# Performance work log

Hardware: AMD Instinct MI355X
Metric: run time of the kernel (lower is better)

The kernel has to match this reference:

```python
import jax, jax.numpy as jnp
import numpy as np

V = 778   # MANO mesh vertex count (hard-coded in the module)
K = 9     # spiral neighborhood length
C = 256   # in_channels
OUT = 3   # out_channels (per-vertex offset xyz)
B3 = 192  # 3 * B, B = 64


def setup_inputs() -> dict:
    key = jax.random.key(0)
    ks = jax.random.split(key, 12)
    x = jax.random.normal(ks[0], (B3, V, C), jnp.float32)
    pred_occ = jax.random.normal(ks[1], (B3, 2, 5), jnp.float32)
    indices = jax.random.randint(ks[2], (V, K), 0, V)
    finger_sizes = [112, 120, 124, 116, 108]
    fingers = {f"finger{i}": jax.random.randint(ks[3 + i], (n,), 0, V)
               for i, n in enumerate(finger_sizes)}

    def lin(k, fan_in, fan_out):
        kw, kb = jax.random.split(k)
        w = jax.random.normal(kw, (fan_in, fan_out), jnp.float32) / np.float32(np.sqrt(fan_in))
        b = jax.random.normal(kb, (fan_out,), jnp.float32) * 0.01
        return w, b

    w0, b0 = lin(ks[8], 2 * C * K, 2 * C)
    w1, b1 = lin(ks[9], 2 * C * K, C)
    w2, b2 = lin(ks[10], C * K, C)
    wh, bh = lin(ks[11], C * K, OUT)
    return {"x": x, "pred_occ": pred_occ, "indices": indices, **fingers,
            "w0": w0, "b0": b0, "w1": w1, "b1": b1, "w2": w2, "b2": b2,
            "wh": wh, "bh": bh}


def spiral_conv(x, idx, w, b):
    # x: [B, V, Cin], idx: [V, K] -> gather spiral neighbors, flatten, linear
    B = x.shape[0]
    g = x[:, idx.reshape(-1), :].reshape(B, V, -1)  # [B, V, K*Cin]
    return g @ w + b


def reference(x, pred_occ, indices, finger0, finger1, finger2, finger3, finger4,
              w0, b0, w1, b1, w2, b2, wh, bh):
    # Per-finger non-occlusion probabilities: softmax over class dim, take class 0
    occ = jax.nn.softmax(pred_occ, axis=1)[:, 0, :5]          # [3B, 5]
    weights = jnp.ones((x.shape[0], V), x.dtype)
    for i, fidx in enumerate([finger0, finger1, finger2, finger3, finger4]):
        val = jnp.broadcast_to(occ[:, i:i + 1], (x.shape[0], fidx.shape[0]))
        weights = weights.at[:, fidx].set(val)
    B = x.shape[0] // 3
    wv = jnp.stack(jnp.split(weights, 3, axis=0), axis=-1)[..., None]  # [B, V, 3, 1]
    wv = jax.nn.softmax(wv, axis=2)
    xv = jnp.stack(jnp.split(x, 3, axis=0), axis=2)                    # [B, V, 3, C]
    wx = jnp.sum(wv * xv, axis=2)                                      # [B, V, C]
    h = jnp.concatenate([wx, x[:B]], axis=2)                           # [B, V, 2C]
    h = jax.nn.relu(spiral_conv(h, indices, w0, b0))
    h = jax.nn.relu(spiral_conv(h, indices, w1, b1))
    h = jax.nn.relu(spiral_conv(h, indices, w2, b2))
    return spiral_conv(h, indices, wh, bh)                             # [B, V, 3]
```

## Files before the change

### kernel.cpp

```cpp
#include <hip/hip_runtime.h>

typedef unsigned short ushort_t;
typedef __attribute__((ext_vector_type(8))) __bf16 bf16x8;
typedef __attribute__((ext_vector_type(8))) unsigned short ushort8;
typedef __attribute__((ext_vector_type(4))) float floatx4;
typedef __attribute__((ext_vector_type(16))) float floatx16;

#define VN 778
#define KNB 9

__device__ __forceinline__ float bf2f(unsigned short s) {
  union { unsigned int u; float f; } x; x.u = ((unsigned int)s) << 16; return x.f;
}
__device__ __forceinline__ unsigned short f2bf(float f) {
  union { float f; unsigned int u; } x; x.f = f;
  unsigned int r = x.u + 0x7fffu + ((x.u >> 16) & 1u);
  return (unsigned short)(r >> 16);
}

__global__ void prep_misc(const float* __restrict__ pred_occ,
                          const int* f0, const int* f1, const int* f2,
                          const int* f3, const int* f4,
                          int n0, int n1, int n2, int n3, int n4,
                          const float* __restrict__ wh,
                          float* __restrict__ occ, int* __restrict__ fid,
                          float* __restrict__ whT) {
  int t = threadIdx.x;
  for (int i = t; i < 192 * 5; i += 256) {
    int r = i / 5, f = i % 5;
    float p0 = pred_occ[r * 10 + f];
    float p1 = pred_occ[r * 10 + 5 + f];
    occ[i] = 1.0f / (1.0f + __expf(p1 - p0));
  }
  for (int i = t; i < VN; i += 256) fid[i] = -1;
  __syncthreads();
  const int* fp[5] = {f0, f1, f2, f3, f4};
  int fn[5] = {n0, n1, n2, n3, n4};
  for (int fi = 0; fi < 5; ++fi) {
    for (int i = t; i < fn[fi]; i += 256) fid[fp[fi][i]] = fi;
    __syncthreads();
  }
  for (int i = t; i < 3 * 2304; i += 256) {
    int o = i / 2304, k = i % 2304;
    whT[i] = wh[k * 3 + o];
  }
}

__global__ void wx_kernel(const float* __restrict__ x, const float* __restrict__ occ,
                          const int* __restrict__ fid, ushort_t* __restrict__ wx) {
  int g = blockIdx.x * 256 + threadIdx.x;
  int c8 = (g & 31) << 3;
  int bv = g >> 5;
  int b = bv / VN;
  int v = bv - b * VN;
  int f = fid[v];
  float w0 = 1.f, w1 = 1.f, w2 = 1.f;
  if (f >= 0) {
    w0 = occ[b * 5 + f];
    w1 = occ[(64 + b) * 5 + f];
    w2 = occ[(128 + b) * 5 + f];
  }
  float m = fmaxf(w0, fmaxf(w1, w2));
  float e0 = __expf(w0 - m), e1 = __expf(w1 - m), e2 = __expf(w2 - m);
  float inv = 1.0f / (e0 + e1 + e2);
  e0 *= inv; e1 *= inv; e2 *= inv;
  size_t base = (size_t)bv * 256 + c8;
  const size_t V1 = (size_t)64 * VN * 256, V2 = (size_t)128 * VN * 256;
  floatx4 x0a = *(const floatx4*)(x + base);
  floatx4 x0b = *(const floatx4*)(x + base + 4);
  floatx4 x1a = *(const floatx4*)(x + V1 + base);
  floatx4 x1b = *(const floatx4*)(x + V1 + base + 4);
  floatx4 x2a = *(const floatx4*)(x + V2 + base);
  floatx4 x2b = *(const floatx4*)(x + V2 + base + 4);
  ushort8 o;
#pragma unroll
  for (int e = 0; e < 4; ++e) {
    o[e]     = f2bf(e0 * x0a[e] + e1 * x1a[e] + e2 * x2a[e]);
    o[e + 4] = f2bf(e0 * x0b[e] + e1 * x1b[e] + e2 * x2b[e]);
  }
  *(ushort8*)(wx + base) = o;
}

__global__ void pack_w(const float* __restrict__ w, ushort_t* __restrict__ wP,
                       int N, int ksn, int total) {
  int chunk = blockIdx.x * 256 + threadIdx.x;
  if (chunk >= total) return;
  int lane = chunk & 63;
  int rest = chunk >> 6;
  int ks = rest % ksn;
  int tn = rest / ksn;
  int n = (tn << 5) + (lane & 31);
  int kb = (ks << 4) + ((lane >> 5) << 3);
  ushort8 o;
#pragma unroll
  for (int j = 0; j < 8; ++j) o[j] = f2bf(w[(size_t)(kb + j) * N + n]);
  *(ushort8*)(wP + (size_t)chunk * 8) = o;
}

template <int CIN, bool SPLIT>
__global__ __launch_bounds__(512, 4) void spiral_gemm(
    const ushort_t* __restrict__ act0, const float* __restrict__ actF,
    const ushort_t* __restrict__ wP, const float* __restrict__ bias,
    const int* __restrict__ idx, ushort_t* __restrict__ out, int NOUT) {
  constexpr int PHASES = CIN / 128;
  __shared__ __align__(16) ushort_t Alds[2 * 64 * 128];
  const int v0 = blockIdx.x * 2;
  const int n0 = blockIdx.y << 8;
  const int tid = threadIdx.x;
  const int lane = tid & 63;
  const int wv = tid >> 6;
  const int vi = wv >> 2;
  const int nq = wv & 3;
  const int mlo = lane & 31;
  const int q = lane >> 5;
  const int xm = mlo & 7;
  floatx16 acc00{}, acc01{}, acc10{}, acc11{};
  const int KtotSteps = KNB * (CIN / 16);
  const int tn0 = (n0 >> 5) + (nq << 1);
  const ushort_t* bp0 = wP + (size_t)tn0 * KtotSteps * 512 + lane * 8;
  const ushort_t* bp1 = bp0 + (size_t)KtotSteps * 512;
  const int* iv0 = idx + v0 * KNB;
  const int* iv1 = idx + (v0 + 1) * KNB;
  const int a_off0 = vi * 64 * 128 + mlo * 128;
  const int a_off1 = vi * 64 * 128 + (mlo + 32) * 128;
  for (int nbr = 0; nbr < KNB; ++nbr) {
    const int nv0 = iv0[nbr], nv1 = iv1[nbr];
#pragma unroll
    for (int h = 0; h < PHASES; ++h) {
      __syncthreads();
#pragma unroll
      for (int it = 0; it < 4; ++it) {
        int L = it * 512 + tid;
        int ck = L & 15;
        int row = (L >> 4) & 63;
        int vv = L >> 10;
        int nv = vv ? nv1 : nv0;
        int c = ck << 3;
        ushort8 val;
        if (SPLIT && h >= 2) {
          const float* src = actF + ((size_t)(row * VN + nv)) * 256 + (h - 2) * 128 + c;
          floatx4 fa = *(const floatx4*)src;
          floatx4 fb = *(const floatx4*)(src + 4);
#pragma unroll
          for (int e = 0; e < 4; ++e) { val[e] = f2bf(fa[e]); val[e + 4] = f2bf(fb[e]); }
        } else {
          const ushort_t* src = act0 + ((size_t)(row * VN + nv)) * (SPLIT ? 256 : CIN)
                                + h * 128 + c;
          val = *(const ushort8*)src;
        }
        int slot = ck ^ (row & 7);
        *(ushort8*)&Alds[(size_t)(vv * 64 * 128) + (size_t)(row * 16 + slot) * 8] = val;
      }
      __syncthreads();
#pragma unroll
      for (int ks = 0; ks < 8; ++ks) {
        int ck0 = ((ks << 1) + q) ^ xm;
        bf16x8 a0 = *(const bf16x8*)&Alds[a_off0 + ck0 * 8];
        bf16x8 a1 = *(const bf16x8*)&Alds[a_off1 + ck0 * 8];
        bf16x8 b0v = *(const bf16x8*)bp0; bp0 += 512;
        bf16x8 b1v = *(const bf16x8*)bp1; bp1 += 512;
        acc00 = __builtin_amdgcn_mfma_f32_32x32x16_bf16(a0, b0v, acc00, 0, 0, 0);
        acc10 = __builtin_amdgcn_mfma_f32_32x32x16_bf16(a1, b0v, acc10, 0, 0, 0);
        acc01 = __builtin_amdgcn_mfma_f32_32x32x16_bf16(a0, b1v, acc01, 0, 0, 0);
        acc11 = __builtin_amdgcn_mfma_f32_32x32x16_bf16(a1, b1v, acc11, 0, 0, 0);
      }
    }
  }
  const int v = v0 + vi;
  const int na = n0 + (nq << 6) + mlo;
  const int nb = na + 32;
  const float ba = bias[na];
  const float bb = bias[nb];
#pragma unroll
  for (int r = 0; r < 16; ++r) {
    int m = (r & 3) + ((r >> 2) << 3) + (q << 2);
    size_t o0 = ((size_t)(m * VN + v)) * NOUT;
    size_t o1 = ((size_t)((m + 32) * VN + v)) * NOUT;
    float v00 = acc00[r] + ba; v00 = v00 > 0.f ? v00 : 0.f;
    float v01 = acc01[r] + bb; v01 = v01 > 0.f ? v01 : 0.f;
    float v10 = acc10[r] + ba; v10 = v10 > 0.f ? v10 : 0.f;
    float v11 = acc11[r] + bb; v11 = v11 > 0.f ? v11 : 0.f;
    out[o0 + na] = f2bf(v00);
    out[o0 + nb] = f2bf(v01);
    out[o1 + na] = f2bf(v10);
    out[o1 + nb] = f2bf(v11);
  }
}

__global__ void head_kernel(const ushort_t* __restrict__ act, const float* __restrict__ whT,
                            const float* __restrict__ bh, const int* __restrict__ idx,
                            float* __restrict__ out) {
  __shared__ __align__(16) ushort_t Alds[64 * 256];
  const int v = blockIdx.x;
  const int tid = threadIdx.x;
  float a0 = 0.f, a1 = 0.f, a2 = 0.f;
  const int b = tid;
  const int xm = b & 7;
  for (int nbr = 0; nbr < KNB; ++nbr) {
    const int nv = idx[v * KNB + nbr];
    __syncthreads();
#pragma unroll
    for (int it = 0; it < 8; ++it) {
      int L = it * 256 + tid;
      int bb = L >> 5;
      int jj = L & 31;
      ushort8 val = *(const ushort8*)(act + ((size_t)(bb * VN + nv)) * 256 + (jj << 3));
      int slot = jj ^ (bb & 7);
      *(ushort8*)&Alds[(size_t)(bb * 32 + slot) * 8] = val;
    }
    __syncthreads();
    if (tid < 64) {
      const float* wp = whT + nbr * 256;
#pragma unroll 4
      for (int j = 0; j < 32; ++j) {
        int jj = j ^ xm;
        ushort8 a8 = *(const ushort8*)&Alds[(b * 32 + jj) * 8];
#pragma unroll
        for (int e = 0; e < 8; ++e) {
          float av = bf2f(a8[e]);
          int k = (j << 3) + e;
          a0 += av * wp[k];
          a1 += av * wp[2304 + k];
          a2 += av * wp[4608 + k];
        }
      }
    }
  }
  if (tid < 64) {
    size_t o = ((size_t)(b * VN + v)) * 3;
    out[o + 0] = a0 + bh[0];
    out[o + 1] = a1 + bh[1];
    out[o + 2] = a2 + bh[2];
  }
}

extern "C" void kernel_launch(void* const* d_in, const int* in_sizes, int n_in,
                              void* d_out, int out_size, void* d_ws, size_t ws_size,
                              hipStream_t stream) {
  const float* x        = (const float*)d_in[0];
  const float* pred_occ = (const float*)d_in[1];
  const int* indices    = (const int*)d_in[2];
  const int* f0 = (const int*)d_in[3];
  const int* f1 = (const int*)d_in[4];
  const int* f2 = (const int*)d_in[5];
  const int* f3 = (const int*)d_in[6];
  const int* f4 = (const int*)d_in[7];
  const float* w0 = (const float*)d_in[8];
  const float* b0 = (const float*)d_in[9];
  const float* w1 = (const float*)d_in[10];
  const float* b1 = (const float*)d_in[11];
  const float* w2 = (const float*)d_in[12];
  const float* b2 = (const float*)d_in[13];
  const float* wh = (const float*)d_in[14];
  const float* bh = (const float*)d_in[15];
  float* outp = (float*)d_out;

  char* ws = (char*)d_ws;
  ushort_t* wP0 = (ushort_t*)(ws + 0);
  ushort_t* wP1 = (ushort_t*)(ws + 4718592);
  ushort_t* wP2 = (ushort_t*)(ws + 7077888);
  float* whT    = (float*)(ws + 8257536);
  float* occ    = (float*)(ws + 8285184);
  int* fid      = (int*)(ws + 8289024);
  ushort_t* R0  = (ushort_t*)(ws + 8292352);
  ushort_t* R1  = (ushort_t*)(ws + 33785856);

  prep_misc<<<1, 256, 0, stream>>>(pred_occ, f0, f1, f2, f3, f4,
                                   in_sizes[3], in_sizes[4], in_sizes[5],
                                   in_sizes[6], in_sizes[7], wh, occ, fid, whT);
  pack_w<<<294912 / 256, 256, 0, stream>>>(w0, wP0, 512, 288, 294912);
  pack_w<<<147456 / 256, 256, 0, stream>>>(w1, wP1, 256, 288, 147456);
  pack_w<<<73728 / 256, 256, 0, stream>>>(w2, wP2, 256, 144, 73728);
  wx_kernel<<<6224, 256, 0, stream>>>(x, occ, fid, R0);

  dim3 g0(VN / 2, 2), g1(VN / 2, 1);
  spiral_gemm<512, true><<<g0, 512, 0, stream>>>(R0, x, wP0, b0, indices, R1, 512);
  spiral_gemm<512, false><<<g1, 512, 0, stream>>>(R1, nullptr, wP1, b1, indices, R0, 256);
  spiral_gemm<256, false><<<g1, 512, 0, stream>>>(R0, nullptr, wP2, b2, indices, R1, 256);
  head_kernel<<<VN, 256, 0, stream>>>(R1, whT, bh, indices, outp);
  (void)n_in; (void)out_size; (void)ws_size;
}
```

Baseline: 1.0000 ms.

## Double-buffer spiral GEMM with direct global-to-LDS loads and pre-converted bf16 input

```diff
diff --git a/kernel.cpp b/kernel.cpp
--- a/kernel.cpp
+++ b/kernel.cpp
@@ -16,6 +16,12 @@
   union { float f; unsigned int u; } x; x.f = f;
   unsigned int r = x.u + 0x7fffu + ((x.u >> 16) & 1u);
   return (unsigned short)(r >> 16);
+}
+
+__device__ __forceinline__ void load_lds16(const void* g, void* l) {
+  __builtin_amdgcn_global_load_lds(
+      (const __attribute__((address_space(1))) unsigned int*)g,
+      (__attribute__((address_space(3))) unsigned int*)l, 16, 0, 0);
 }
 
 __global__ void prep_misc(const float* __restrict__ pred_occ,
@@ -81,6 +87,17 @@
   *(ushort8*)(wx + base) = o;
 }
 
+__global__ void xcvt_kernel(const float* __restrict__ x, ushort_t* __restrict__ xb) {
+  int g = blockIdx.x * 256 + threadIdx.x;
+  size_t base = (size_t)g * 8;
+  floatx4 fa = *(const floatx4*)(x + base);
+  floatx4 fb = *(const floatx4*)(x + base + 4);
+  ushort8 o;
+#pragma unroll
+  for (int e = 0; e < 4; ++e) { o[e] = f2bf(fa[e]); o[e + 4] = f2bf(fb[e]); }
+  *(ushort8*)(xb + base) = o;
+}
+
 __global__ void pack_w(const float* __restrict__ w, ushort_t* __restrict__ wP,
                        int N, int ksn, int total) {
   int chunk = blockIdx.x * 256 + threadIdx.x;
@@ -97,93 +114,113 @@
   *(ushort8*)(wP + (size_t)chunk * 8) = o;
 }
 
-template <int CIN, bool SPLIT>
+template <int CIN, int MODE>
 __global__ __launch_bounds__(512, 4) void spiral_gemm(
     const ushort_t* __restrict__ act0, const float* __restrict__ actF,
-    const ushort_t* __restrict__ wP, const float* __restrict__ bias,
-    const int* __restrict__ idx, ushort_t* __restrict__ out, int NOUT) {
-  constexpr int PHASES = CIN / 128;
-  __shared__ __align__(16) ushort_t Alds[2 * 64 * 128];
+    const ushort_t* __restrict__ actB, const ushort_t* __restrict__ wP,
+    const float* __restrict__ bias, const int* __restrict__ idx,
+    ushort_t* __restrict__ out, int NOUT) {
+  constexpr int H = CIN / 128;
+  constexpr int P = KNB * H;
+  __shared__ __align__(16) ushort_t Alds[2][2048 * 8];
   const int v0 = blockIdx.x * 2;
   const int n0 = blockIdx.y << 8;
   const int tid = threadIdx.x;
   const int lane = tid & 63;
   const int wv = tid >> 6;
-  const int vi = wv >> 2;
-  const int nq = wv & 3;
   const int mlo = lane & 31;
   const int q = lane >> 5;
   const int xm = mlo & 7;
-  floatx16 acc00{}, acc01{}, acc10{}, acc11{};
+  floatx16 acc0{}, acc1{}, acc2{}, acc3{};
   const int KtotSteps = KNB * (CIN / 16);
-  const int tn0 = (n0 >> 5) + (nq << 1);
-  const ushort_t* bp0 = wP + (size_t)tn0 * KtotSteps * 512 + lane * 8;
-  const ushort_t* bp1 = bp0 + (size_t)KtotSteps * 512;
+  const int tn0 = (n0 >> 5) + wv;
+  const ushort_t* bp = wP + (size_t)tn0 * KtotSteps * 512 + lane * 8;
   const int* iv0 = idx + v0 * KNB;
-  const int* iv1 = idx + (v0 + 1) * KNB;
-  const int a_off0 = vi * 64 * 128 + mlo * 128;
-  const int a_off1 = vi * 64 * 128 + (mlo + 32) * 128;
-  for (int nbr = 0; nbr < KNB; ++nbr) {
-    const int nv0 = iv0[nbr], nv1 = iv1[nbr];
-#pragma unroll
-    for (int h = 0; h < PHASES; ++h) {
-      __syncthreads();
-#pragma unroll
-      for (int it = 0; it < 4; ++it) {
-        int L = it * 512 + tid;
-        int ck = L & 15;
-        int row = (L >> 4) & 63;
-        int vv = L >> 10;
-        int nv = vv ? nv1 : nv0;
-        int c = ck << 3;
-        ushort8 val;
-        if (SPLIT && h >= 2) {
-          const float* src = actF + ((size_t)(row * VN + nv)) * 256 + (h - 2) * 128 + c;
-          floatx4 fa = *(const floatx4*)src;
-          floatx4 fb = *(const floatx4*)(src + 4);
-#pragma unroll
-          for (int e = 0; e < 4; ++e) { val[e] = f2bf(fa[e]); val[e + 4] = f2bf(fb[e]); }
-        } else {
-          const ushort_t* src = act0 + ((size_t)(row * VN + nv)) * (SPLIT ? 256 : CIN)
-                                + h * 128 + c;
-          val = *(const ushort8*)src;
-        }
-        int slot = ck ^ (row & 7);
-        *(ushort8*)&Alds[(size_t)(vv * 64 * 128) + (size_t)(row * 16 + slot) * 8] = val;
+  const int* iv1 = iv0 + KNB;
+  const int aoff0 = mlo * 128;
+  const int aoff1 = (mlo + 32) * 128;
+  const int aoff2 = 8192 + mlo * 128;
+  const int aoff3 = 8192 + (mlo + 32) * 128;
+
+  auto dma_stage = [&](int p, ushort_t* buf) {
+    const int nbr = p / H, h = p - nbr * H;
+    const int nva = iv0[nbr], nvb = iv1[nbr];
+#pragma unroll
+    for (int it = 0; it < 4; ++it) {
+      const int slotb = ((wv << 2) + it) << 6;
+      const int s = slotb + lane;
+      const int vv = s >> 10;
+      const int row = (s >> 4) & 63;
+      const int ck = (s & 15) ^ (row & 7);
+      const int nv = vv ? nvb : nva;
+      const ushort_t* src;
+      if (MODE == 0) {
+        src = act0 + ((size_t)(row * VN + nv)) * CIN + h * 128 + ck * 8;
+      } else {
+        const ushort_t* basep = (MODE == 1 || h < 2) ? act0 : actB;
+        src = basep + ((size_t)(row * VN + nv)) * 256 + (h & 1) * 128 + ck * 8;
       }
-      __syncthreads();
-#pragma unroll
-      for (int ks = 0; ks < 8; ++ks) {
-        int ck0 = ((ks << 1) + q) ^ xm;
-        bf16x8 a0 = *(const bf16x8*)&Alds[a_off0 + ck0 * 8];
-        bf16x8 a1 = *(const bf16x8*)&Alds[a_off1 + ck0 * 8];
-        bf16x8 b0v = *(const bf16x8*)bp0; bp0 += 512;
-        bf16x8 b1v = *(const bf16x8*)bp1; bp1 += 512;
-        acc00 = __builtin_amdgcn_mfma_f32_32x32x16_bf16(a0, b0v, acc00, 0, 0, 0);
-        acc10 = __builtin_amdgcn_mfma_f32_32x32x16_bf16(a1, b0v, acc10, 0, 0, 0);
-        acc01 = __builtin_amdgcn_mfma_f32_32x32x16_bf16(a0, b1v, acc01, 0, 0, 0);
-        acc11 = __builtin_amdgcn_mfma_f32_32x32x16_bf16(a1, b1v, acc11, 0, 0, 0);
-      }
-    }
-  }
-  const int v = v0 + vi;
-  const int na = n0 + (nq << 6) + mlo;
-  const int nb = na + 32;
-  const float ba = bias[na];
-  const float bb = bias[nb];
-#pragma unroll
-  for (int r = 0; r < 16; ++r) {
-    int m = (r & 3) + ((r >> 2) << 3) + (q << 2);
-    size_t o0 = ((size_t)(m * VN + v)) * NOUT;
-    size_t o1 = ((size_t)((m + 32) * VN + v)) * NOUT;
-    float v00 = acc00[r] + ba; v00 = v00 > 0.f ? v00 : 0.f;
-    float v01 = acc01[r] + bb; v01 = v01 > 0.f ? v01 : 0.f;
-    float v10 = acc10[r] + ba; v10 = v10 > 0.f ? v10 : 0.f;
-    float v11 = acc11[r] + bb; v11 = v11 > 0.f ? v11 : 0.f;
-    out[o0 + na] = f2bf(v00);
-    out[o0 + nb] = f2bf(v01);
-    out[o1 + na] = f2bf(v10);
-    out[o1 + nb] = f2bf(v11);
+      load_lds16(src, buf + (size_t)slotb * 8);
+    }
+  };
+  auto f32_stage = [&](int p, ushort_t* buf) {
+    const int nbr = p / H, h = p - nbr * H;
+    const int nva = iv0[nbr], nvb = iv1[nbr];
+#pragma unroll
+    for (int j = 0; j < 4; ++j) {
+      const int s = (j << 9) + tid;
+      const int vv = s >> 10;
+      const int row = (s >> 4) & 63;
+      const int ck = (s & 15) ^ (row & 7);
+      const int nv = vv ? nvb : nva;
+      const float* src = actF + ((size_t)(row * VN + nv)) * 256 + (h - 2) * 128 + ck * 8;
+      floatx4 fa = *(const floatx4*)src;
+      floatx4 fb = *(const floatx4*)(src + 4);
+      ushort8 o;
+#pragma unroll
+      for (int e = 0; e < 4; ++e) { o[e] = f2bf(fa[e]); o[e + 4] = f2bf(fb[e]); }
+      *(ushort8*)(buf + (size_t)s * 8) = o;
+    }
+  };
+
+  dma_stage(0, Alds[0]);
+  __syncthreads();
+#pragma unroll 2
+  for (int p = 0; p < P; ++p) {
+    ushort_t* cur = Alds[p & 1];
+    ushort_t* nxt = Alds[(p + 1) & 1];
+    const bool have_next = (p + 1 < P);
+    const bool next_f32 = (MODE == 1) && (((p + 1) & (H - 1)) >= 2);
+    if (have_next && !next_f32) dma_stage(p + 1, nxt);
+#pragma unroll
+    for (int ks = 0; ks < 8; ++ks) {
+      const int cko = ((((ks << 1) + q) ^ xm) << 3);
+      bf16x8 a0 = *(const bf16x8*)(cur + aoff0 + cko);
+      bf16x8 a1 = *(const bf16x8*)(cur + aoff1 + cko);
+      bf16x8 a2 = *(const bf16x8*)(cur + aoff2 + cko);
+      bf16x8 a3 = *(const bf16x8*)(cur + aoff3 + cko);
+      bf16x8 bv = *(const bf16x8*)bp; bp += 512;
+      acc0 = __builtin_amdgcn_mfma_f32_32x32x16_bf16(a0, bv, acc0, 0, 0, 0);
+      acc1 = __builtin_amdgcn_mfma_f32_32x32x16_bf16(a1, bv, acc1, 0, 0, 0);
+      acc2 = __builtin_amdgcn_mfma_f32_32x32x16_bf16(a2, bv, acc2, 0, 0, 0);
+      acc3 = __builtin_amdgcn_mfma_f32_32x32x16_bf16(a3, bv, acc3, 0, 0, 0);
+    }
+    __syncthreads();
+    if (have_next && next_f32) { f32_stage(p + 1, nxt); __syncthreads(); }
+  }
+  const int n = n0 + (wv << 5) + mlo;
+  const float bn = bias[n];
+#pragma unroll
+  for (int t = 0; t < 4; ++t) {
+    const floatx16 av = (t == 0) ? acc0 : (t == 1) ? acc1 : (t == 2) ? acc2 : acc3;
+    const int vcur = v0 + (t >> 1);
+    const int bbase = (t & 1) << 5;
+#pragma unroll
+    for (int r = 0; r < 16; ++r) {
+      const int m = (r & 3) + ((r >> 2) << 3) + (q << 2);
+      float val = av[r] + bn; val = val > 0.f ? val : 0.f;
+      out[((size_t)((bbase + m) * VN + vcur)) * NOUT + n] = f2bf(val);
+    }
   }
 }
 
@@ -264,6 +301,8 @@
   int* fid      = (int*)(ws + 8289024);
   ushort_t* R0  = (ushort_t*)(ws + 8292352);
   ushort_t* R1  = (ushort_t*)(ws + 33785856);
+  ushort_t* XB  = (ushort_t*)(ws + 84772864);
+  const bool useXB = (ws_size >= 110266368ull);
 
   prep_misc<<<1, 256, 0, stream>>>(pred_occ, f0, f1, f2, f3, f4,
                                    in_sizes[3], in_sizes[4], in_sizes[5],
@@ -271,12 +310,19 @@
   pack_w<<<294912 / 256, 256, 0, stream>>>(w0, wP0, 512, 288, 294912);
   pack_w<<<147456 / 256, 256, 0, stream>>>(w1, wP1, 256, 288, 147456);
   pack_w<<<73728 / 256, 256, 0, stream>>>(w2, wP2, 256, 144, 73728);
+  if (useXB) xcvt_kernel<<<6224, 256, 0, stream>>>(x, XB);
   wx_kernel<<<6224, 256, 0, stream>>>(x, occ, fid, R0);
 
-  dim3 g0(VN / 2, 2), g1(VN / 2, 1);
-  spiral_gemm<512, true><<<g0, 512, 0, stream>>>(R0, x, wP0, b0, indices, R1, 512);
-  spiral_gemm<512, false><<<g1, 512, 0, stream>>>(R1, nullptr, wP1, b1, indices, R0, 256);
-  spiral_gemm<256, false><<<g1, 512, 0, stream>>>(R0, nullptr, wP2, b2, indices, R1, 256);
+  if (useXB)
+    spiral_gemm<512, 2><<<dim3(389, 2), 512, 0, stream>>>(R0, nullptr, XB, wP0, b0,
+                                                          indices, R1, 512);
+  else
+    spiral_gemm<512, 1><<<dim3(389, 2), 512, 0, stream>>>(R0, x, nullptr, wP0, b0,
+                                                          indices, R1, 512);
+  spiral_gemm<512, 0><<<dim3(389, 1), 512, 0, stream>>>(R1, nullptr, nullptr, wP1, b1,
+                                                        indices, R0, 256);
+  spiral_gemm<256, 0><<<dim3(389, 1), 512, 0, stream>>>(R0, nullptr, nullptr, wP2, b2,
+                                                        indices, R1, 256);
   head_kernel<<<VN, 256, 0, stream>>>(R1, whT, bh, indices, outp);
-  (void)n_in; (void)out_size; (void)ws_size;
-}
+  (void)n_in; (void)out_size;
+}
```

New measurement: 852.7 us. -14.7%, faster.
